# Kernel tuning notes

Measured on AMD Instinct MI355X. Metric: run time of the kernel, lower is better.

Reference implementation:

```python
import jax, jax.numpy as jnp
import numpy as np

# Forward-arg scalars from the original torch signature (mixed-kappa branch):
KAPPA = 0.5          # 0 < kappa < 1 -> exercises C, V, grad, corr_loss, whit_loss
# compute_grad=True, compute_loss=True, batched=False


def setup_inputs() -> dict:
    key = jax.random.key(0)
    x = jax.random.normal(key, (8, 4096, 1024), dtype=jnp.float32)  # (b, l, d)
    return {"x": x}


def reference(x):
    # batched=False: flatten (b, l, d) -> (M, d)
    b, l, d = x.shape
    xf = x.reshape(b * l, d)                      # (M, d)
    M = xf.shape[0]

    # mean outer product over samples: (1/M) * X^T X, instead of
    # materializing the huge (M, d, d) broadcast tensor the torch code builds.
    mean_outer = jnp.einsum('mi,mj->ij', xf, xf) / M   # (d, d)
    eye = jnp.eye(d, dtype=x.dtype)
    mean_C = mean_outer * (1.0 - eye)             # diagonal zeroed (mean of C)
    mean_V = jnp.mean(xf * xf, axis=0) - 1.0      # (d,) mean of diag(C) - 1

    # grad = mean over M of [(1-kappa)*C  with  diag += kappa*V]
    grad = (1.0 - KAPPA) * mean_C + KAPPA * jnp.diag(mean_V)

    # corr_loss = mean over (M, d, d) of C*C with zeroed diagonal:
    #   sum_{i!=j} (x_i x_j)^2 = (sum_i x_i^2)^2 - sum_i x_i^4 per sample
    sq = xf * xf                                  # (M, d)
    sum_sq = jnp.sum(sq, axis=-1)                 # (M,)
    sum_quart = jnp.sum(sq * sq, axis=-1)         # (M,)
    corr_loss = jnp.mean(sum_sq * sum_sq - sum_quart) / (d * d)

    # whit_loss = mean((x^2 - 1)^2)
    whit_loss = jnp.mean((sq - 1.0) ** 2)

    return grad, corr_loss, whit_loss
```

## Files before the change

kernel.cpp:

```cpp
#include <hip/hip_runtime.h>
#include <hip/hip_bf16.h>
#include <stdint.h>
#include <stddef.h>


#define D_DIM 1024
#define M_ROWS 32768
#define BK 128
#define NKBS (M_ROWS / BK)
#define NTILES 36
#define TILE_ELEMS 16384
#define CP_U32 8192

typedef __attribute__((ext_vector_type(4))) float f32x4;
typedef __attribute__((ext_vector_type(4))) int i32x4;
typedef __attribute__((ext_vector_type(8))) int i32x8;

__device__ inline unsigned short f2bf(float f) {
  unsigned int b = __float_as_uint(f);
  return (unsigned short)((b + 0x7fffu + ((b >> 16) & 1u)) >> 16);
}

__device__ inline void gload_lds16(const void* g, void* l) {
  __builtin_amdgcn_global_load_lds(
      (const __attribute__((address_space(1))) void*)g,
      (__attribute__((address_space(3))) void*)l,
      16, 0, 0);
}

__global__ __launch_bounds__(256) void k_pass1(const float* __restrict__ x,
                                               unsigned char* __restrict__ xt,
                                               float* __restrict__ rssp,
                                               float* __restrict__ rs4p) {
  __shared__ unsigned int sh32[16 * 68];
  const int bid = blockIdx.x;
  const int m0 = (bid & 511) * 64;
  const int ct = bid >> 9;
  const int c0 = ct * 64;
  const int t = (int)threadIdx.x;
  const int q = t >> 4;
  const int cg = t & 15;

  unsigned int p[4];
  float ss[4], s4[4];
#pragma unroll
  for (int mi = 0; mi < 4; ++mi) {
    const float4 v = *(const float4*)(x + (size_t)(m0 + q * 4 + mi) * D_DIM + c0 + cg * 4);
    const float q0 = v.x * v.x, q1 = v.y * v.y, q2 = v.z * v.z, q3 = v.w * v.w;
    ss[mi] = q0 + q1 + q2 + q3;
    s4[mi] = q0 * q0 + q1 * q1 + q2 * q2 + q3 * q3;
    unsigned int u = (unsigned int)__builtin_amdgcn_cvt_pk_fp8_f32(v.x, v.y, 0, false);
    p[mi] = (unsigned int)__builtin_amdgcn_cvt_pk_fp8_f32(v.z, v.w, (int)u, true);
  }
#pragma unroll
  for (int off = 8; off; off >>= 1) {
#pragma unroll
    for (int mi = 0; mi < 4; ++mi) {
      ss[mi] += __shfl_xor(ss[mi], off, 16);
      s4[mi] += __shfl_xor(s4[mi], off, 16);
    }
  }
  if (cg == 0) {
#pragma unroll
    for (int mi = 0; mi < 4; ++mi) {
      rssp[ct * M_ROWS + m0 + q * 4 + mi] = ss[mi];
      rs4p[ct * M_ROWS + m0 + q * 4 + mi] = s4[mi];
    }
  }

  const unsigned int t01l = __builtin_amdgcn_perm(p[1], p[0], 0x05010400u);
  const unsigned int t01h = __builtin_amdgcn_perm(p[1], p[0], 0x07030602u);
  const unsigned int t23l = __builtin_amdgcn_perm(p[3], p[2], 0x05010400u);
  const unsigned int t23h = __builtin_amdgcn_perm(p[3], p[2], 0x07030602u);
  uint4 w;
  w.x = __builtin_amdgcn_perm(t23l, t01l, 0x05040100u);
  w.y = __builtin_amdgcn_perm(t23l, t01l, 0x07060302u);
  w.z = __builtin_amdgcn_perm(t23h, t01h, 0x05040100u);
  w.w = __builtin_amdgcn_perm(t23h, t01h, 0x07060302u);
  *(uint4*)&sh32[q * 68 + cg * 4] = w;
  __syncthreads();

  const int c = t >> 2, mh = t & 3;
  uint4 o;
  o.x = sh32[(mh * 4 + 0) * 68 + c];
  o.y = sh32[(mh * 4 + 1) * 68 + c];
  o.z = sh32[(mh * 4 + 2) * 68 + c];
  o.w = sh32[(mh * 4 + 3) * 68 + c];
  *(uint4*)(xt + ((size_t)(c0 + c) << 15) + m0 + mh * 16) = o;
}

__global__ __launch_bounds__(256) void k_gemm(const unsigned char* __restrict__ xt,
                                              unsigned int* __restrict__ cpart,
                                              int S, int swz) {
  __shared__ unsigned char As[2][16384];
  __shared__ unsigned char Bs[2][16384];
  const int bid = (int)blockIdx.x;
  int s, tidx;
  if (swz) {
    const int xcd = bid & 7;
    tidx = (bid >> 3) % NTILES;
    s = (bid / (8 * NTILES)) * 8 + xcd;
  } else {
    s = bid / NTILES;
    tidx = bid - s * NTILES;
  }
  int rem = tidx, ti = 0;
  while (rem >= 8 - ti) { rem -= 8 - ti; ++ti; }
  const int tj = ti + rem;
  const bool diag = (ti == tj);

  const int t = (int)threadIdx.x;
  const int l = t & 63, w = t >> 6;
  const int wr = w >> 1, wc = w & 1;
  const int r = l & 15, g = l >> 4;

  f32x4 acc[4][4];
#pragma unroll
  for (int mi = 0; mi < 4; ++mi)
#pragma unroll
    for (int ni = 0; ni < 4; ++ni) acc[mi][ni] = (f32x4){0.f, 0.f, 0.f, 0.f};

  const int srow = t >> 3;
  const int sl = (((t & 7) ^ (srow & 7)) << 4);
  const unsigned char* pa[4];
  const unsigned char* pb[4];
#pragma unroll
  for (int j = 0; j < 4; ++j) {
    pa[j] = xt + ((size_t)(ti * 128 + j * 32 + srow) << 15) + sl;
    pb[j] = xt + ((size_t)(tj * 128 + j * 32 + srow) << 15) + sl;
  }

#define STAGE(B, K) do { \
    _Pragma("unroll") \
    for (int j = 0; j < 4; ++j) { \
      gload_lds16(pa[j] + (K), &As[B][j * 4096 + t * 16]); \
      if (!diag) gload_lds16(pb[j] + (K), &Bs[B][j * 4096 + t * 16]); \
    } \
  } while (0)

  const int swb = r & 7;
  const int oA0 = (((2 * g + 0) ^ swb) << 4);
  const int oA1 = (((2 * g + 1) ^ swb) << 4);
  const int arow = (wr * 64 + r) * 128;
  const int brow = (wc * 64 + r) * 128;

#define COMPUTE(B, DS, SB, KN) do { \
    i32x4 alo[4], ahi[4], blo[4], bhi[4]; \
    const unsigned char* Ab = As[B]; \
    const unsigned char* Bb = diag ? As[B] : Bs[B]; \
    _Pragma("unroll") \
    for (int mi = 0; mi < 4; ++mi) { \
      alo[mi] = *(const i32x4*)(Ab + arow + mi * 2048 + oA0); \
      ahi[mi] = *(const i32x4*)(Ab + arow + mi * 2048 + oA1); \
      blo[mi] = *(const i32x4*)(Bb + brow + mi * 2048 + oA0); \
      bhi[mi] = *(const i32x4*)(Bb + brow + mi * 2048 + oA1); \
    } \
    if (DS) STAGE(SB, KN); \
    i32x8 a8[4], b8[4]; \
    _Pragma("unroll") \
    for (int mi = 0; mi < 4; ++mi) { \
      a8[mi] = (i32x8){alo[mi][0], alo[mi][1], alo[mi][2], alo[mi][3], \
                       ahi[mi][0], ahi[mi][1], ahi[mi][2], ahi[mi][3]}; \
      b8[mi] = (i32x8){blo[mi][0], blo[mi][1], blo[mi][2], blo[mi][3], \
                       bhi[mi][0], bhi[mi][1], bhi[mi][2], bhi[mi][3]}; \
    } \
    _Pragma("unroll") \
    for (int mi = 0; mi < 4; ++mi) \
      _Pragma("unroll") \
      for (int ni = 0; ni < 4; ++ni) \
        acc[mi][ni] = __builtin_amdgcn_mfma_scale_f32_16x16x128_f8f6f4( \
            a8[mi], b8[ni], acc[mi][ni], 0, 0, 0, 0x7F7F7F7Fu, 0, 0x7F7F7F7Fu); \
    __syncthreads(); \
  } while (0)

  const int kq = NKBS / S, kr = NKBS - kq * S;
  const int kb0 = s * kq + (s < kr ? s : kr);
  const int nkb = kq + (s < kr ? 1 : 0);
  size_t k = (size_t)kb0 * BK;

  STAGE(0, k);
  __syncthreads();
  int it = 0;
  for (; it + 2 <= nkb; it += 2) {
    COMPUTE(0, 1, 1, k + BK);
    COMPUTE(1, (it + 2 < nkb), 0, k + 2 * BK);
    k += 2 * BK;
  }
  if (it < nkb) COMPUTE(0, 0, 0, 0);

#undef STAGE
#undef COMPUTE

  unsigned int* cp = cpart + ((size_t)s * NTILES + tidx) * CP_U32;
#pragma unroll
  for (int mi = 0; mi < 4; ++mi) {
    const int rowb = wr * 64 + mi * 16 + g * 4;
#pragma unroll
    for (int ni = 0; ni < 4; ++ni) {
      const int col = wc * 64 + ni * 16 + r;
      const unsigned int w0 = (unsigned int)f2bf(acc[mi][ni][0]) |
                              ((unsigned int)f2bf(acc[mi][ni][1]) << 16);
      const unsigned int w1 = (unsigned int)f2bf(acc[mi][ni][2]) |
                              ((unsigned int)f2bf(acc[mi][ni][3]) << 16);
      cp[(size_t)((rowb >> 1) + 0) * 128 + col] = w0;
      cp[(size_t)((rowb >> 1) + 1) * 128 + col] = w1;
    }
  }
}

__global__ __launch_bounds__(256) void k_epi1(const unsigned int* __restrict__ cpart,
                                              float* __restrict__ csum, int S) {
  const int i4 = ((int)blockIdx.x * 256 + (int)threadIdx.x) * 4;
  float lo0 = 0.f, lo1 = 0.f, lo2 = 0.f, lo3 = 0.f;
  float hi0 = 0.f, hi1 = 0.f, hi2 = 0.f, hi3 = 0.f;
  for (int s = 0; s < S; ++s) {
    const uint4 v = *(const uint4*)(cpart + (size_t)s * (NTILES * CP_U32) + i4);
    lo0 += __uint_as_float(v.x << 16); hi0 += __uint_as_float(v.x & 0xFFFF0000u);
    lo1 += __uint_as_float(v.y << 16); hi1 += __uint_as_float(v.y & 0xFFFF0000u);
    lo2 += __uint_as_float(v.z << 16); hi2 += __uint_as_float(v.z & 0xFFFF0000u);
    lo3 += __uint_as_float(v.w << 16); hi3 += __uint_as_float(v.w & 0xFFFF0000u);
  }
  const int tile = i4 >> 13;
  const int qq = i4 & (CP_U32 - 1);
  const int rp = qq >> 7, c = qq & 127;
  float* base = csum + (size_t)tile * TILE_ELEMS + (size_t)(2 * rp) * 128 + c;
  float4 a; a.x = lo0; a.y = lo1; a.z = lo2; a.w = lo3;
  float4 b; b.x = hi0; b.y = hi1; b.z = hi2; b.w = hi3;
  *(float4*)base = a;
  *(float4*)(base + 128) = b;
}

__global__ __launch_bounds__(256) void k_epi2(const float* __restrict__ csum,
                                              float* __restrict__ out) {
  const int idx = (int)blockIdx.x * 256 + (int)threadIdx.x;
  const int i = idx >> 8;
  const int j0 = (idx & 255) * 4;
  const int ti = i >> 7, tj = j0 >> 7;
  const float sc = 0.5f / (float)M_ROWS;
  float4 o;
  if (ti <= tj) {
    const int src = ti * 8 - (ti * (ti - 1)) / 2 + tj - ti;
    const float4 v = *(const float4*)(csum + (size_t)src * TILE_ELEMS +
                                      (size_t)(i & 127) * 128 + (j0 & 127));
    o.x = v.x * sc; o.y = v.y * sc; o.z = v.z * sc; o.w = v.w * sc;
    if (i >= j0 && i < j0 + 4) {
      const float cd = (i == j0) ? v.x : (i == j0 + 1) ? v.y : (i == j0 + 2) ? v.z : v.w;
      const float dv = 0.5f * (cd / (float)M_ROWS - 1.0f);
      if (i == j0) o.x = dv; else if (i == j0 + 1) o.y = dv;
      else if (i == j0 + 2) o.z = dv; else o.w = dv;
    }
  } else {
    const int src = tj * 8 - (tj * (tj - 1)) / 2 + ti - tj;
    const int jj = j0 & 127, ii = i & 127;
    const float* base = csum + (size_t)src * TILE_ELEMS + ii;
    o.x = base[(size_t)(jj + 0) * 128] * sc;
    o.y = base[(size_t)(jj + 1) * 128] * sc;
    o.z = base[(size_t)(jj + 2) * 128] * sc;
    o.w = base[(size_t)(jj + 3) * 128] * sc;
  }
  *(float4*)(out + (size_t)i * D_DIM + j0) = o;
}

__global__ __launch_bounds__(256) void k_fin1(const float* __restrict__ rssp,
                                              const float* __restrict__ rs4p,
                                              float* __restrict__ scp) {
  __shared__ float sm[3][4];
  const int t = (int)threadIdx.x;
  const int m = (int)blockIdx.x * 256 + t;
  float a = 0.f, b = 0.f;
#pragma unroll
  for (int ct = 0; ct < 16; ++ct) {
    a += rssp[ct * M_ROWS + m];
    b += rs4p[ct * M_ROWS + m];
  }
  float corr = a * a - b;
#pragma unroll
  for (int off = 32; off; off >>= 1) {
    corr += __shfl_down(corr, off);
    a += __shfl_down(a, off);
    b += __shfl_down(b, off);
  }
  const int wv = t >> 6;
  if ((t & 63) == 0) { sm[0][wv] = corr; sm[1][wv] = a; sm[2][wv] = b; }
  __syncthreads();
  if (t == 0) {
    float c4 = 0.f, a4 = 0.f, b4 = 0.f;
#pragma unroll
    for (int i = 0; i < 4; ++i) { c4 += sm[0][i]; a4 += sm[1][i]; b4 += sm[2][i]; }
    scp[(int)blockIdx.x * 4 + 0] = c4;
    scp[(int)blockIdx.x * 4 + 1] = a4;
    scp[(int)blockIdx.x * 4 + 2] = b4;
  }
}

__global__ __launch_bounds__(128) void k_fin2(const float* __restrict__ scp,
                                              float* __restrict__ out) {
  __shared__ float sm[3][2];
  const int t = (int)threadIdx.x;
  float c = scp[t * 4 + 0], a = scp[t * 4 + 1], b = scp[t * 4 + 2];
#pragma unroll
  for (int off = 32; off; off >>= 1) {
    c += __shfl_down(c, off);
    a += __shfl_down(a, off);
    b += __shfl_down(b, off);
  }
  const int wv = t >> 6;
  if ((t & 63) == 0) { sm[0][wv] = c; sm[1][wv] = a; sm[2][wv] = b; }
  __syncthreads();
  if (t == 0) {
    const double ct = (double)sm[0][0] + (double)sm[0][1];
    const double st = (double)sm[1][0] + (double)sm[1][1];
    const double qt = (double)sm[2][0] + (double)sm[2][1];
    const double N = (double)M_ROWS * (double)D_DIM;
    out[1048576] = (float)(ct / (double)M_ROWS / ((double)D_DIM * (double)D_DIM));
    out[1048577] = (float)((qt - 2.0 * st + N) / N);
  }
}

extern "C" void kernel_launch(void* const* d_in, const int* in_sizes, int n_in,
                              void* d_out, int out_size, void* d_ws, size_t ws_size,
                              hipStream_t stream) {
  (void)in_sizes; (void)n_in; (void)out_size;
  const float* x = (const float*)d_in[0];
  float* out = (float*)d_out;
  char* ws = (char*)d_ws;

  unsigned char* xt = (unsigned char*)ws;
  float* rssp = (float*)(ws + 33554432);
  float* rs4p = (float*)(ws + 35651584);
  float* scp  = (float*)(ws + 37748736);
  float* csum = (float*)(ws + 37752832);
  unsigned int* cpart = (unsigned int*)(ws + 40112128);
  const size_t base = 40112128;
  size_t avail = (ws_size > base) ? (ws_size - base) : 0;
  int S = (int)(avail / (sizeof(unsigned int) * NTILES * CP_U32));
  if (S > 32) S = 32;
  int swz = 0;
  if (S >= 8) { S &= ~7; swz = 1; }
  if (S < 1) S = 1;

  k_pass1<<<8192, 256, 0, stream>>>(x, xt, rssp, rs4p);
  k_gemm<<<NTILES * S, 256, 0, stream>>>(xt, cpart, S, swz);
  k_epi1<<<288, 256, 0, stream>>>(cpart, csum, S);
  k_epi2<<<1024, 256, 0, stream>>>(csum, out);
  k_fin1<<<128, 256, 0, stream>>>(rssp, rs4p, scp);
  k_fin2<<<1, 128, 0, stream>>>(scp, out);
}
```

Before: 85.07 us.

## Fuse split-K reduction with symmetric output scatter and widen pass1 transpose tiles

Merges the two epilogue kernels into one that reduces the bf16 split-K partials and writes the upper tile plus its mirrored transpose directly to the output through shared memory. This removes the intermediate csum buffer and one kernel launch. Pass1 now handles 256 rows per block with 64-byte contiguous fp8 stores instead of 16-byte ones, and the partial-sum loop is unrolled by four to keep more loads in flight. The price is a larger LDS footprint in pass1 and a shared-memory transpose step in the epilogue.

```diff
diff --git a/kernel.cpp b/kernel.cpp
--- a/kernel.cpp
+++ b/kernel.cpp
@@ -32,61 +32,69 @@
                                                unsigned char* __restrict__ xt,
                                                float* __restrict__ rssp,
                                                float* __restrict__ rs4p) {
-  __shared__ unsigned int sh32[16 * 68];
+  __shared__ unsigned int sh[64 * 68];
   const int bid = blockIdx.x;
-  const int m0 = (bid & 511) * 64;
-  const int ct = bid >> 9;
+  const int m0 = (bid & 127) * 256;
+  const int ct = bid >> 7;
   const int c0 = ct * 64;
   const int t = (int)threadIdx.x;
-  const int q = t >> 4;
-  const int cg = t & 15;
-
-  unsigned int p[4];
-  float ss[4], s4[4];
-#pragma unroll
-  for (int mi = 0; mi < 4; ++mi) {
-    const float4 v = *(const float4*)(x + (size_t)(m0 + q * 4 + mi) * D_DIM + c0 + cg * 4);
-    const float q0 = v.x * v.x, q1 = v.y * v.y, q2 = v.z * v.z, q3 = v.w * v.w;
-    ss[mi] = q0 + q1 + q2 + q3;
-    s4[mi] = q0 * q0 + q1 * q1 + q2 * q2 + q3 * q3;
-    unsigned int u = (unsigned int)__builtin_amdgcn_cvt_pk_fp8_f32(v.x, v.y, 0, false);
-    p[mi] = (unsigned int)__builtin_amdgcn_cvt_pk_fp8_f32(v.z, v.w, (int)u, true);
-  }
-#pragma unroll
-  for (int off = 8; off; off >>= 1) {
-#pragma unroll
-    for (int mi = 0; mi < 4; ++mi) {
-      ss[mi] += __shfl_xor(ss[mi], off, 16);
-      s4[mi] += __shfl_xor(s4[mi], off, 16);
+  const int mg = t >> 2;
+  const int cs = t & 3;
+
+  float ss[4] = {0.f, 0.f, 0.f, 0.f};
+  float s4[4] = {0.f, 0.f, 0.f, 0.f};
+  const float* xb = x + (size_t)(m0 + mg * 4) * D_DIM + c0 + cs * 16;
+
+#pragma unroll
+  for (int cg = 0; cg < 4; ++cg) {
+    unsigned int p[4];
+#pragma unroll
+    for (int ri = 0; ri < 4; ++ri) {
+      const float4 v = *(const float4*)(xb + (size_t)ri * D_DIM + cg * 4);
+      const float q0 = v.x * v.x, q1 = v.y * v.y, q2 = v.z * v.z, q3 = v.w * v.w;
+      ss[ri] += q0 + q1 + q2 + q3;
+      s4[ri] += q0 * q0 + q1 * q1 + q2 * q2 + q3 * q3;
+      unsigned int u = (unsigned int)__builtin_amdgcn_cvt_pk_fp8_f32(v.x, v.y, 0, false);
+      p[ri] = (unsigned int)__builtin_amdgcn_cvt_pk_fp8_f32(v.z, v.w, (int)u, true);
     }
-  }
-  if (cg == 0) {
-#pragma unroll
-    for (int mi = 0; mi < 4; ++mi) {
-      rssp[ct * M_ROWS + m0 + q * 4 + mi] = ss[mi];
-      rs4p[ct * M_ROWS + m0 + q * 4 + mi] = s4[mi];
+    const unsigned int t01l = __builtin_amdgcn_perm(p[1], p[0], 0x05010400u);
+    const unsigned int t01h = __builtin_amdgcn_perm(p[1], p[0], 0x07030602u);
+    const unsigned int t23l = __builtin_amdgcn_perm(p[3], p[2], 0x05010400u);
+    const unsigned int t23h = __builtin_amdgcn_perm(p[3], p[2], 0x07030602u);
+    const int cbase = (cs * 16 + cg * 4) * 68 + mg;
+    sh[cbase + 0 * 68] = __builtin_amdgcn_perm(t23l, t01l, 0x05040100u);
+    sh[cbase + 1 * 68] = __builtin_amdgcn_perm(t23l, t01l, 0x07060302u);
+    sh[cbase + 2 * 68] = __builtin_amdgcn_perm(t23h, t01h, 0x05040100u);
+    sh[cbase + 3 * 68] = __builtin_amdgcn_perm(t23h, t01h, 0x07060302u);
+  }
+
+#pragma unroll
+  for (int ri = 0; ri < 4; ++ri) {
+    ss[ri] += __shfl_xor(ss[ri], 1, 4);
+    ss[ri] += __shfl_xor(ss[ri], 2, 4);
+    s4[ri] += __shfl_xor(s4[ri], 1, 4);
+    s4[ri] += __shfl_xor(s4[ri], 2, 4);
+  }
+  if (cs == 0) {
+#pragma unroll
+    for (int ri = 0; ri < 4; ++ri) {
+      rssp[ct * M_ROWS + m0 + mg * 4 + ri] = ss[ri];
+      rs4p[ct * M_ROWS + m0 + mg * 4 + ri] = s4[ri];
     }
   }
-
-  const unsigned int t01l = __builtin_amdgcn_perm(p[1], p[0], 0x05010400u);
-  const unsigned int t01h = __builtin_amdgcn_perm(p[1], p[0], 0x07030602u);
-  const unsigned int t23l = __builtin_amdgcn_perm(p[3], p[2], 0x05010400u);
-  const unsigned int t23h = __builtin_amdgcn_perm(p[3], p[2], 0x07030602u);
-  uint4 w;
-  w.x = __builtin_amdgcn_perm(t23l, t01l, 0x05040100u);
-  w.y = __builtin_amdgcn_perm(t23l, t01l, 0x07060302u);
-  w.z = __builtin_amdgcn_perm(t23h, t01h, 0x05040100u);
-  w.w = __builtin_amdgcn_perm(t23h, t01h, 0x07060302u);
-  *(uint4*)&sh32[q * 68 + cg * 4] = w;
   __syncthreads();
 
-  const int c = t >> 2, mh = t & 3;
-  uint4 o;
-  o.x = sh32[(mh * 4 + 0) * 68 + c];
-  o.y = sh32[(mh * 4 + 1) * 68 + c];
-  o.z = sh32[(mh * 4 + 2) * 68 + c];
-  o.w = sh32[(mh * 4 + 3) * 68 + c];
-  *(uint4*)(xt + ((size_t)(c0 + c) << 15) + m0 + mh * 16) = o;
+  const int c = t >> 2, ch = t & 3;
+  const unsigned int* sp = &sh[c * 68 + ch * 16];
+  const uint4 o0 = *(const uint4*)(sp + 0);
+  const uint4 o1 = *(const uint4*)(sp + 4);
+  const uint4 o2 = *(const uint4*)(sp + 8);
+  const uint4 o3 = *(const uint4*)(sp + 12);
+  unsigned char* dst = xt + ((size_t)(c0 + c) << 15) + m0 + ch * 64;
+  *(uint4*)(dst + 0) = o0;
+  *(uint4*)(dst + 16) = o1;
+  *(uint4*)(dst + 32) = o2;
+  *(uint4*)(dst + 48) = o3;
 }
 
 __global__ __launch_bounds__(256) void k_gemm(const unsigned char* __restrict__ xt,
@@ -208,57 +216,85 @@
   }
 }
 
-__global__ __launch_bounds__(256) void k_epi1(const unsigned int* __restrict__ cpart,
-                                              float* __restrict__ csum, int S) {
-  const int i4 = ((int)blockIdx.x * 256 + (int)threadIdx.x) * 4;
+__global__ __launch_bounds__(256) void k_epi(const unsigned int* __restrict__ cpart,
+                                             float* __restrict__ out, int S) {
+  __shared__ float smir[16][132];
+  const int b = (int)blockIdx.x;
+  const int tile = b >> 3, chunk = b & 7;
+  int rem = tile, ti = 0;
+  while (rem >= 8 - ti) { rem -= 8 - ti; ++ti; }
+  const int tj = ti + rem;
+  const int t = (int)threadIdx.x;
+  const int i4 = (b * 256 + t) * 4;
+  const int rpl = t >> 5;
+  const int c = (t & 31) * 4;
+
+  const unsigned int* cp = cpart + i4;
+  const size_t st = (size_t)NTILES * CP_U32;
   float lo0 = 0.f, lo1 = 0.f, lo2 = 0.f, lo3 = 0.f;
   float hi0 = 0.f, hi1 = 0.f, hi2 = 0.f, hi3 = 0.f;
-  for (int s = 0; s < S; ++s) {
-    const uint4 v = *(const uint4*)(cpart + (size_t)s * (NTILES * CP_U32) + i4);
+  int s = 0;
+  for (; s + 4 <= S; s += 4) {
+    const uint4 v0 = *(const uint4*)(cp + (size_t)(s + 0) * st);
+    const uint4 v1 = *(const uint4*)(cp + (size_t)(s + 1) * st);
+    const uint4 v2 = *(const uint4*)(cp + (size_t)(s + 2) * st);
+    const uint4 v3 = *(const uint4*)(cp + (size_t)(s + 3) * st);
+    lo0 += __uint_as_float(v0.x << 16); hi0 += __uint_as_float(v0.x & 0xFFFF0000u);
+    lo1 += __uint_as_float(v0.y << 16); hi1 += __uint_as_float(v0.y & 0xFFFF0000u);
+    lo2 += __uint_as_float(v0.z << 16); hi2 += __uint_as_float(v0.z & 0xFFFF0000u);
+    lo3 += __uint_as_float(v0.w << 16); hi3 += __uint_as_float(v0.w & 0xFFFF0000u);
+    lo0 += __uint_as_float(v1.x << 16); hi0 += __uint_as_float(v1.x & 0xFFFF0000u);
+    lo1 += __uint_as_float(v1.y << 16); hi1 += __uint_as_float(v1.y & 0xFFFF0000u);
+    lo2 += __uint_as_float(v1.z << 16); hi2 += __uint_as_float(v1.z & 0xFFFF0000u);
+    lo3 += __uint_as_float(v1.w << 16); hi3 += __uint_as_float(v1.w & 0xFFFF0000u);
+    lo0 += __uint_as_float(v2.x << 16); hi0 += __uint_as_float(v2.x & 0xFFFF0000u);
+    lo1 += __uint_as_float(v2.y << 16); hi1 += __uint_as_float(v2.y & 0xFFFF0000u);
+    lo2 += __uint_as_float(v2.z << 16); hi2 += __uint_as_float(v2.z & 0xFFFF0000u);
+    lo3 += __uint_as_float(v2.w << 16); hi3 += __uint_as_float(v2.w & 0xFFFF0000u);
+    lo0 += __uint_as_float(v3.x << 16); hi0 += __uint_as_float(v3.x & 0xFFFF0000u);
+    lo1 += __uint_as_float(v3.y << 16); hi1 += __uint_as_float(v3.y & 0xFFFF0000u);
+    lo2 += __uint_as_float(v3.z << 16); hi2 += __uint_as_float(v3.z & 0xFFFF0000u);
+    lo3 += __uint_as_float(v3.w << 16); hi3 += __uint_as_float(v3.w & 0xFFFF0000u);
+  }
+  for (; s < S; ++s) {
+    const uint4 v = *(const uint4*)(cp + (size_t)s * st);
     lo0 += __uint_as_float(v.x << 16); hi0 += __uint_as_float(v.x & 0xFFFF0000u);
     lo1 += __uint_as_float(v.y << 16); hi1 += __uint_as_float(v.y & 0xFFFF0000u);
     lo2 += __uint_as_float(v.z << 16); hi2 += __uint_as_float(v.z & 0xFFFF0000u);
     lo3 += __uint_as_float(v.w << 16); hi3 += __uint_as_float(v.w & 0xFFFF0000u);
   }
-  const int tile = i4 >> 13;
-  const int qq = i4 & (CP_U32 - 1);
-  const int rp = qq >> 7, c = qq & 127;
-  float* base = csum + (size_t)tile * TILE_ELEMS + (size_t)(2 * rp) * 128 + c;
-  float4 a; a.x = lo0; a.y = lo1; a.z = lo2; a.w = lo3;
-  float4 b; b.x = hi0; b.y = hi1; b.z = hi2; b.w = hi3;
-  *(float4*)base = a;
-  *(float4*)(base + 128) = b;
-}
-
-__global__ __launch_bounds__(256) void k_epi2(const float* __restrict__ csum,
-                                              float* __restrict__ out) {
-  const int idx = (int)blockIdx.x * 256 + (int)threadIdx.x;
-  const int i = idx >> 8;
-  const int j0 = (idx & 255) * 4;
-  const int ti = i >> 7, tj = j0 >> 7;
+
   const float sc = 0.5f / (float)M_ROWS;
-  float4 o;
-  if (ti <= tj) {
-    const int src = ti * 8 - (ti * (ti - 1)) / 2 + tj - ti;
-    const float4 v = *(const float4*)(csum + (size_t)src * TILE_ELEMS +
-                                      (size_t)(i & 127) * 128 + (j0 & 127));
-    o.x = v.x * sc; o.y = v.y * sc; o.z = v.z * sc; o.w = v.w * sc;
-    if (i >= j0 && i < j0 + 4) {
-      const float cd = (i == j0) ? v.x : (i == j0 + 1) ? v.y : (i == j0 + 2) ? v.z : v.w;
-      const float dv = 0.5f * (cd / (float)M_ROWS - 1.0f);
-      if (i == j0) o.x = dv; else if (i == j0 + 1) o.y = dv;
-      else if (i == j0 + 2) o.z = dv; else o.w = dv;
+  f32x4 lo = (f32x4){lo0 * sc, lo1 * sc, lo2 * sc, lo3 * sc};
+  f32x4 hi = (f32x4){hi0 * sc, hi1 * sc, hi2 * sc, hi3 * sc};
+
+  const int gi = ti * 128 + chunk * 16 + 2 * rpl;
+  const int gj = tj * 128 + c;
+  if (ti == tj) {
+#pragma unroll
+    for (int kk = 0; kk < 4; ++kk) {
+      if (gi == gj + kk) lo[kk] -= 0.5f;
+      if (gi + 1 == gj + kk) hi[kk] -= 0.5f;
     }
-  } else {
-    const int src = tj * 8 - (tj * (tj - 1)) / 2 + ti - tj;
-    const int jj = j0 & 127, ii = i & 127;
-    const float* base = csum + (size_t)src * TILE_ELEMS + ii;
-    o.x = base[(size_t)(jj + 0) * 128] * sc;
-    o.y = base[(size_t)(jj + 1) * 128] * sc;
-    o.z = base[(size_t)(jj + 2) * 128] * sc;
-    o.w = base[(size_t)(jj + 3) * 128] * sc;
-  }
-  *(float4*)(out + (size_t)i * D_DIM + j0) = o;
+  }
+  *(f32x4*)(out + (size_t)gi * D_DIM + gj) = lo;
+  *(f32x4*)(out + (size_t)(gi + 1) * D_DIM + gj) = hi;
+
+  if (ti != tj) {
+    const int jr = 2 * rpl;
+    *(f32x4*)&smir[jr][c] = lo;
+    *(f32x4*)&smir[jr + 1][c] = hi;
+    __syncthreads();
+    const int cc = t >> 1, j0 = (t & 1) * 8;
+    f32x4 m0v, m1v;
+    m0v[0] = smir[j0 + 0][cc]; m0v[1] = smir[j0 + 1][cc];
+    m0v[2] = smir[j0 + 2][cc]; m0v[3] = smir[j0 + 3][cc];
+    m1v[0] = smir[j0 + 4][cc]; m1v[1] = smir[j0 + 5][cc];
+    m1v[2] = smir[j0 + 6][cc]; m1v[3] = smir[j0 + 7][cc];
+    float* ob = out + (size_t)(tj * 128 + cc) * D_DIM + ti * 128 + chunk * 16 + j0;
+    *(f32x4*)(ob + 0) = m0v;
+    *(f32x4*)(ob + 4) = m1v;
+  }
 }
 
 __global__ __launch_bounds__(256) void k_fin1(const float* __restrict__ rssp,
@@ -329,9 +365,8 @@
   float* rssp = (float*)(ws + 33554432);
   float* rs4p = (float*)(ws + 35651584);
   float* scp  = (float*)(ws + 37748736);
-  float* csum = (float*)(ws + 37752832);
-  unsigned int* cpart = (unsigned int*)(ws + 40112128);
-  const size_t base = 40112128;
+  unsigned int* cpart = (unsigned int*)(ws + 37752832);
+  const size_t base = 37752832;
   size_t avail = (ws_size > base) ? (ws_size - base) : 0;
   int S = (int)(avail / (sizeof(unsigned int) * NTILES * CP_U32));
   if (S > 32) S = 32;
@@ -339,10 +374,9 @@
   if (S >= 8) { S &= ~7; swz = 1; }
   if (S < 1) S = 1;
 
-  k_pass1<<<8192, 256, 0, stream>>>(x, xt, rssp, rs4p);
+  k_pass1<<<2048, 256, 0, stream>>>(x, xt, rssp, rs4p);
   k_gemm<<<NTILES * S, 256, 0, stream>>>(xt, cpart, S, swz);
-  k_epi1<<<288, 256, 0, stream>>>(cpart, csum, S);
-  k_epi2<<<1024, 256, 0, stream>>>(csum, out);
+  k_epi<<<288, 256, 0, stream>>>(cpart, out, S);
   k_fin1<<<128, 256, 0, stream>>>(rssp, rs4p, scp);
   k_fin2<<<1, 128, 0, stream>>>(scp, out);
 }
```

New measurement: 88.20 us. +3.7%, slower.
